# Performance work log

Hardware: AMD Instinct MI355X
Metric: run time of the kernel (lower is better)

## Reference

```python
import jax, jax.numpy as jnp
import numpy as np

B, C, N = 4, 192, 4096
K = 16                      # avg degree
E = B * N * K               # 262144 edges
C_OUT = 384


def setup_inputs() -> dict:
    key = jax.random.key(0)
    k1, k2, k3, k4 = jax.random.split(key, 4)
    x = jax.random.normal(k1, (B, C, N, 1), dtype=jnp.float32)
    edge_index = jax.random.randint(k2, (2, E), 0, B * N, dtype=jnp.int64)
    # BasicConv([2C, C_OUT]): 1x1 Conv2d + bias + ReLU (norm=None)
    W = jax.random.normal(k3, (C_OUT, 2 * C), dtype=jnp.float32) * (1.0 / np.sqrt(2 * C))
    b = jax.random.normal(k4, (C_OUT,), dtype=jnp.float32) * 0.01
    return {"x": x, "edge_index": edge_index, "W": W, "b": b}


def reference(x, edge_index, W, b):
    Bs, Cs, Ns, _ = x.shape
    BN = Bs * Ns
    # (B,C,N,1) -> flattened node table (B*N, C); node id = b*N + n
    x_flat = jnp.transpose(x[..., 0], (0, 2, 1)).reshape(BN, Cs)
    x_i = x_flat[edge_index[0]]          # (E, C) gather at dst
    x_j = x_flat[edge_index[1]]          # (E, C) gather at src
    diff = x_j - x_i
    # scatter-max over dst nodes; torch_scatter fills empty segments with 0
    agg = jax.ops.segment_max(diff, edge_index[0], num_segments=BN)
    agg = jnp.where(jnp.isfinite(agg), agg, 0.0)
    x_j_out = jnp.transpose(agg.reshape(Bs, Ns, Cs), (0, 2, 1))[..., None]  # (B,C,N,1)
    # interleave channels: cat along new axis 2 then reshape -> (B, 2C, N, 1)
    cat = jnp.stack([x, x_j_out], axis=2).reshape(Bs, 2 * Cs, Ns, 1)
    # 1x1 conv == GEMM over channels, + bias + ReLU
    out = jnp.einsum('oc,bcnw->bonw', W, cat) + b[None, :, None, None]
    return jax.nn.relu(out)
```

## Files before the change

### kernel.cpp

```cpp
#include <hip/hip_runtime.h>
#include <hip/hip_bf16.h>
#include <math.h>

#define Bz    4
#define Cch   192
#define Nn    4096
#define BN    16384
#define Ecnt  262144
#define COUT  384
#define CAP   64
#define MSTR  200

typedef __attribute__((ext_vector_type(8))) short short8;
typedef __attribute__((ext_vector_type(4))) float floatx4;

__device__ __forceinline__ float b2f(unsigned short u) {
    union { unsigned int i; float f; } z; z.i = ((unsigned int)u) << 16; return z.f;
}
__device__ __forceinline__ unsigned short f2b(float f) {
    __hip_bfloat16 h = __float2bfloat16(f);
    return *(unsigned short*)&h;
}

#define RED8(mm, FLD) do {                                                    \
    float a_ = fmaxf(fmaxf(b2f(v[0].FLD), b2f(v[1].FLD)),                     \
                     fmaxf(b2f(v[2].FLD), b2f(v[3].FLD)));                    \
    float b_ = fmaxf(fmaxf(b2f(v[4].FLD), b2f(v[5].FLD)),                     \
                     fmaxf(b2f(v[6].FLD), b2f(v[7].FLD)));                    \
    mm = fmaxf(mm, fmaxf(a_, b_)); } while (0)

__global__ __launch_bounds__(256) void prep_kernel(
    const float* __restrict__ x, const unsigned int* __restrict__ ew,
    const float* __restrict__ W, __hip_bfloat16* __restrict__ xb,
    __hip_bfloat16* __restrict__ Wxa, __hip_bfloat16* __restrict__ Wa,
    int* __restrict__ deg, int* __restrict__ flag) {
    int bid = blockIdx.x;
    if (bid < 3072) {
        __shared__ float tile[32][33];
        int b = bid / 768;
        int r = bid - b * 768;
        int c0 = (r >> 7) * 32;
        int n0 = (r & 127) * 32;
        int tx = threadIdx.x & 31, ty = threadIdx.x >> 5;
        for (int i = ty; i < 32; i += 8)
            tile[i][tx] = x[((size_t)(b * Cch + c0 + i)) * Nn + n0 + tx];
        __syncthreads();
        for (int i = ty; i < 32; i += 8)
            xb[((size_t)(b * Nn + n0 + i)) * Cch + c0 + tx] =
                __float2bfloat16(tile[tx][i]);
    } else if (bid < 3360) {
        int i = (bid - 3072) * 256 + threadIdx.x;
        int o = i / Cch, c = i - o * Cch;
        float wx = W[o * 2 * Cch + 2 * c];
        float wa = W[o * 2 * Cch + 2 * c + 1];
        Wxa[i] = __float2bfloat16(wx - wa);
        Wa[i]  = __float2bfloat16(wa);
    } else if (bid < 3424) {
        deg[(bid - 3360) * 256 + threadIdx.x] = 0;
    } else {
        __shared__ int s;
        if (threadIdx.x == 0) s = 1;
        __syncthreads();
        if (ew[2 * threadIdx.x + 1] != 0u) atomicAnd(&s, 0);
        __syncthreads();
        if (threadIdx.x == 0) *flag = s;
    }
}

__global__ __launch_bounds__(256) void fill_kernel(
    const int* __restrict__ ew, const int* __restrict__ flag,
    int* __restrict__ deg, int* __restrict__ slots) {
    int t = blockIdx.x * 256 + threadIdx.x;
    int d0, d1, s0, s1;
    if (*flag) {
        int4 dv = *(const int4*)&ew[4 * t];
        int4 sv = *(const int4*)&ew[2 * Ecnt + 4 * t];
        d0 = dv.x; d1 = dv.z; s0 = sv.x; s1 = sv.z;
    } else {
        int2 dv = *(const int2*)&ew[2 * t];
        int2 sv = *(const int2*)&ew[Ecnt + 2 * t];
        d0 = dv.x; d1 = dv.y; s0 = sv.x; s1 = sv.y;
    }
    int p0 = atomicAdd(&deg[d0], 1); if (p0 < CAP) slots[(d0 << 6) + p0] = s0;
    int p1 = atomicAdd(&deg[d1], 1); if (p1 < CAP) slots[(d1 << 6) + p1] = s1;
}

#define MFMA6()                                                                \
    acc00 = __builtin_amdgcn_mfma_f32_16x16x32_bf16(b0, af0, acc00, 0, 0, 0);  \
    acc10 = __builtin_amdgcn_mfma_f32_16x16x32_bf16(b0, af1, acc10, 0, 0, 0);  \
    acc01 = __builtin_amdgcn_mfma_f32_16x16x32_bf16(b1, af0, acc01, 0, 0, 0);  \
    acc11 = __builtin_amdgcn_mfma_f32_16x16x32_bf16(b1, af1, acc11, 0, 0, 0);  \
    acc02 = __builtin_amdgcn_mfma_f32_16x16x32_bf16(b2, af0, acc02, 0, 0, 0);  \
    acc12 = __builtin_amdgcn_mfma_f32_16x16x32_bf16(b2, af1, acc12, 0, 0, 0)

__global__ __launch_bounds__(512, 4) void p2_kernel(
    const int* __restrict__ deg, const int* __restrict__ slots,
    const __hip_bfloat16* __restrict__ xb,
    const __hip_bfloat16* __restrict__ Wxa, const __hip_bfloat16* __restrict__ Wa,
    const float* __restrict__ bias, float* __restrict__ out)
{
    __shared__ __align__(16) unsigned short Xs[32 * MSTR];
    __shared__ __align__(16) unsigned short Ms[32 * MSTR];
    int tid = threadIdx.x, bid = blockIdx.x;
    int lane = tid & 63, wave = tid >> 6;
    int quad = lane >> 4, lrow = lane & 15;
    int node0 = bid * 32;
    const unsigned short* xbu = (const unsigned short*)xb;
    int act = lane < 48;
    int cb = lane * 4;

    for (int nl = wave * 4; nl < wave * 4 + 4; nl++) {
        int node = node0 + nl;
        int d = deg[node]; if (d > CAP) d = CAP;
        d = __builtin_amdgcn_readfirstlane(d);
        int nbrval = 0;
        if (lane < d) nbrval = slots[(node << 6) + lane];
        ushort4 xv = {0, 0, 0, 0};
        if (act) xv = *(const ushort4*)&xbu[node * Cch + cb];
        float m0 = -INFINITY, m1 = -INFINITY, m2 = -INFINITY, m3 = -INFINITY;
        int k = 0;
        for (; k + 8 <= d; k += 8) {
            int s[8];
#pragma unroll
            for (int u = 0; u < 8; u++) s[u] = __builtin_amdgcn_readlane(nbrval, k + u);
            if (act) {
                ushort4 v[8];
#pragma unroll
                for (int u = 0; u < 8; u++) v[u] = *(const ushort4*)&xbu[s[u] * Cch + cb];
                RED8(m0, x); RED8(m1, y); RED8(m2, z); RED8(m3, w);
            }
        }
        if (k + 4 <= d) {
            int s0 = __builtin_amdgcn_readlane(nbrval, k);
            int s1 = __builtin_amdgcn_readlane(nbrval, k + 1);
            int s2 = __builtin_amdgcn_readlane(nbrval, k + 2);
            int s3 = __builtin_amdgcn_readlane(nbrval, k + 3);
            if (act) {
                ushort4 v0 = *(const ushort4*)&xbu[s0 * Cch + cb];
                ushort4 v1 = *(const ushort4*)&xbu[s1 * Cch + cb];
                ushort4 v2 = *(const ushort4*)&xbu[s2 * Cch + cb];
                ushort4 v3 = *(const ushort4*)&xbu[s3 * Cch + cb];
                m0 = fmaxf(m0, fmaxf(fmaxf(b2f(v0.x), b2f(v1.x)), fmaxf(b2f(v2.x), b2f(v3.x))));
                m1 = fmaxf(m1, fmaxf(fmaxf(b2f(v0.y), b2f(v1.y)), fmaxf(b2f(v2.y), b2f(v3.y))));
                m2 = fmaxf(m2, fmaxf(fmaxf(b2f(v0.z), b2f(v1.z)), fmaxf(b2f(v2.z), b2f(v3.z))));
                m3 = fmaxf(m3, fmaxf(fmaxf(b2f(v0.w), b2f(v1.w)), fmaxf(b2f(v2.w), b2f(v3.w))));
            }
            k += 4;
        }
        for (; k < d; k++) {
            int s = __builtin_amdgcn_readlane(nbrval, k);
            if (act) {
                ushort4 v = *(const ushort4*)&xbu[s * Cch + cb];
                m0 = fmaxf(m0, b2f(v.x)); m1 = fmaxf(m1, b2f(v.y));
                m2 = fmaxf(m2, b2f(v.z)); m3 = fmaxf(m3, b2f(v.w));
            }
        }
        if (act) {
            *(ushort4*)&Xs[nl * MSTR + cb] = xv;
            ushort4 o4;
            if (d > 0) {
                o4.x = f2b(m0); o4.y = f2b(m1); o4.z = f2b(m2); o4.w = f2b(m3);
            } else {
                o4 = xv;
            }
            *(ushort4*)&Ms[nl * MSTR + cb] = o4;
        }
    }
    __syncthreads();

    floatx4 acc00 = {}, acc01 = {}, acc02 = {}, acc10 = {}, acc11 = {}, acc12 = {};
    const unsigned short* Wx16 = (const unsigned short*)Wxa;
    const unsigned short* Wa16 = (const unsigned short*)Wa;
    size_t w0 = (size_t)(wave * 48 +  0 + lrow) * Cch;
    size_t w1 = (size_t)(wave * 48 + 16 + lrow) * Cch;
    size_t w2 = (size_t)(wave * 48 + 32 + lrow) * Cch;
    int kq = quad * 8;

    short8 b0 = *(const short8*)&Wx16[w0 + kq];
    short8 b1 = *(const short8*)&Wx16[w1 + kq];
    short8 b2 = *(const short8*)&Wx16[w2 + kq];
#pragma unroll
    for (int s = 0; s < 12; s++) {
        short8 n0, n1, n2;
        if (s < 11) {
            int sn = s + 1;
            const unsigned short* Wn = (sn >= 6) ? Wa16 : Wx16;
            int kkn = ((sn >= 6) ? sn - 6 : sn) * 32 + kq;
            n0 = *(const short8*)&Wn[w0 + kkn];
            n1 = *(const short8*)&Wn[w1 + kkn];
            n2 = *(const short8*)&Wn[w2 + kkn];
        }
        int kk = ((s >= 6) ? s - 6 : s) * 32 + kq;
        const unsigned short* Ar = (s >= 6) ? Ms : Xs;
        short8 af0 = *(const short8*)&Ar[lrow * MSTR + kk];
        short8 af1 = *(const short8*)&Ar[(16 + lrow) * MSTR + kk];
        MFMA6();
        if (s < 11) { b0 = n0; b1 = n1; b2 = n2; }
    }

    floatx4 accs[2][3] = {{acc00, acc01, acc02}, {acc10, acc11, acc12}};
#pragma unroll
    for (int i = 0; i < 2; i++) {
        int node = node0 + i * 16 + lrow;
        int b = node >> 12, n = node & 4095;
#pragma unroll
        for (int j = 0; j < 3; j++) {
            int ob = wave * 48 + j * 16 + quad * 4;
#pragma unroll
            for (int r = 0; r < 4; r++) {
                int o = ob + r;
                float v = accs[i][j][r] + bias[o];
                out[((size_t)(b * COUT + o)) * Nn + n] = fmaxf(v, 0.0f);
            }
        }
    }
}

extern "C" void kernel_launch(void* const* d_in, const int* in_sizes, int n_in,
                              void* d_out, int out_size, void* d_ws, size_t ws_size,
                              hipStream_t stream) {
    const float* x    = (const float*)d_in[0];
    const int*   ew   = (const int*)d_in[1];
    const float* W    = (const float*)d_in[2];
    const float* bias = (const float*)d_in[3];
    float* out        = (float*)d_out;

    char* ws = (char*)d_ws;
    __hip_bfloat16* xb   = (__hip_bfloat16*)ws;
    __hip_bfloat16* Wxa  = (__hip_bfloat16*)(ws + 12582912);
    __hip_bfloat16* Wa   = (__hip_bfloat16*)(ws + 12730368);
    int* deg   = (int*)(ws + 12877824);
    int* slots = (int*)(ws + 12943360);
    int* flag  = (int*)(ws + 17137664);

    prep_kernel<<<3425, 256, 0, stream>>>(x, (const unsigned int*)ew, W, xb, Wxa, Wa, deg, flag);
    fill_kernel<<<Ecnt / 512, 256, 0, stream>>>(ew, flag, deg, slots);
    p2_kernel<<<BN / 32, 512, 0, stream>>>(deg, slots, xb, Wxa, Wa, bias, out);
}
```

Baseline: 123.2 us.

## Halve nodes per block, prefetch neighbor lists, pick edge dtype on host

The fused gather-max plus GEMM kernel now handles 16 nodes per block instead of 32, doubling the grid to 1024 blocks with half the LDS and a single MFMA row tile per wave. Each wave loads both nodes' degree and neighbor lists up front, so those latencies overlap before the gather loop starts. The on-device int64/int32 flag detection is replaced by a host-side check on the input byte size, which selects a specialised fill kernel and removes the flag read and its branch. The trade-off is that every block now reloads the full weight matrix for only 16 nodes, doubling weight traffic per output.

```diff
diff --git a/kernel.cpp b/kernel.cpp
--- a/kernel.cpp
+++ b/kernel.cpp
@@ -30,10 +30,9 @@
     mm = fmaxf(mm, fmaxf(a_, b_)); } while (0)
 
 __global__ __launch_bounds__(256) void prep_kernel(
-    const float* __restrict__ x, const unsigned int* __restrict__ ew,
-    const float* __restrict__ W, __hip_bfloat16* __restrict__ xb,
-    __hip_bfloat16* __restrict__ Wxa, __hip_bfloat16* __restrict__ Wa,
-    int* __restrict__ deg, int* __restrict__ flag) {
+    const float* __restrict__ x, const float* __restrict__ W,
+    __hip_bfloat16* __restrict__ xb, __hip_bfloat16* __restrict__ Wxa,
+    __hip_bfloat16* __restrict__ Wa, int* __restrict__ deg) {
     int bid = blockIdx.x;
     if (bid < 3072) {
         __shared__ float tile[32][33];
@@ -55,43 +54,35 @@
         float wa = W[o * 2 * Cch + 2 * c + 1];
         Wxa[i] = __float2bfloat16(wx - wa);
         Wa[i]  = __float2bfloat16(wa);
-    } else if (bid < 3424) {
+    } else {
         deg[(bid - 3360) * 256 + threadIdx.x] = 0;
-    } else {
-        __shared__ int s;
-        if (threadIdx.x == 0) s = 1;
-        __syncthreads();
-        if (ew[2 * threadIdx.x + 1] != 0u) atomicAnd(&s, 0);
-        __syncthreads();
-        if (threadIdx.x == 0) *flag = s;
-    }
-}
-
-__global__ __launch_bounds__(256) void fill_kernel(
-    const int* __restrict__ ew, const int* __restrict__ flag,
-    int* __restrict__ deg, int* __restrict__ slots) {
-    int t = blockIdx.x * 256 + threadIdx.x;
-    int d0, d1, s0, s1;
-    if (*flag) {
-        int4 dv = *(const int4*)&ew[4 * t];
-        int4 sv = *(const int4*)&ew[2 * Ecnt + 4 * t];
-        d0 = dv.x; d1 = dv.z; s0 = sv.x; s1 = sv.z;
-    } else {
-        int2 dv = *(const int2*)&ew[2 * t];
-        int2 sv = *(const int2*)&ew[Ecnt + 2 * t];
-        d0 = dv.x; d1 = dv.y; s0 = sv.x; s1 = sv.y;
-    }
+    }
+}
+
+__device__ __forceinline__ void fill_body(
+    int d0, int d1, int s0, int s1, int* deg, int* slots) {
     int p0 = atomicAdd(&deg[d0], 1); if (p0 < CAP) slots[(d0 << 6) + p0] = s0;
     int p1 = atomicAdd(&deg[d1], 1); if (p1 < CAP) slots[(d1 << 6) + p1] = s1;
 }
-
-#define MFMA6()                                                                \
-    acc00 = __builtin_amdgcn_mfma_f32_16x16x32_bf16(b0, af0, acc00, 0, 0, 0);  \
-    acc10 = __builtin_amdgcn_mfma_f32_16x16x32_bf16(b0, af1, acc10, 0, 0, 0);  \
-    acc01 = __builtin_amdgcn_mfma_f32_16x16x32_bf16(b1, af0, acc01, 0, 0, 0);  \
-    acc11 = __builtin_amdgcn_mfma_f32_16x16x32_bf16(b1, af1, acc11, 0, 0, 0);  \
-    acc02 = __builtin_amdgcn_mfma_f32_16x16x32_bf16(b2, af0, acc02, 0, 0, 0);  \
-    acc12 = __builtin_amdgcn_mfma_f32_16x16x32_bf16(b2, af1, acc12, 0, 0, 0)
+__global__ __launch_bounds__(256) void fill64_kernel(
+    const int* __restrict__ ew, int* __restrict__ deg, int* __restrict__ slots) {
+    int t = blockIdx.x * 256 + threadIdx.x;
+    int4 dv = *(const int4*)&ew[4 * t];
+    int4 sv = *(const int4*)&ew[2 * Ecnt + 4 * t];
+    fill_body(dv.x, dv.z, sv.x, sv.z, deg, slots);
+}
+__global__ __launch_bounds__(256) void fill32_kernel(
+    const int* __restrict__ ew, int* __restrict__ deg, int* __restrict__ slots) {
+    int t = blockIdx.x * 256 + threadIdx.x;
+    int2 dv = *(const int2*)&ew[2 * t];
+    int2 sv = *(const int2*)&ew[Ecnt + 2 * t];
+    fill_body(dv.x, dv.y, sv.x, sv.y, deg, slots);
+}
+
+#define MFMA3()                                                                \
+    acc0 = __builtin_amdgcn_mfma_f32_16x16x32_bf16(b0, af0, acc0, 0, 0, 0);    \
+    acc1 = __builtin_amdgcn_mfma_f32_16x16x32_bf16(b1, af0, acc1, 0, 0, 0);    \
+    acc2 = __builtin_amdgcn_mfma_f32_16x16x32_bf16(b2, af0, acc2, 0, 0, 0)
 
 __global__ __launch_bounds__(512, 4) void p2_kernel(
     const int* __restrict__ deg, const int* __restrict__ slots,
@@ -99,22 +90,29 @@
     const __hip_bfloat16* __restrict__ Wxa, const __hip_bfloat16* __restrict__ Wa,
     const float* __restrict__ bias, float* __restrict__ out)
 {
-    __shared__ __align__(16) unsigned short Xs[32 * MSTR];
-    __shared__ __align__(16) unsigned short Ms[32 * MSTR];
+    __shared__ __align__(16) unsigned short Xs[16 * MSTR];
+    __shared__ __align__(16) unsigned short Ms[16 * MSTR];
     int tid = threadIdx.x, bid = blockIdx.x;
     int lane = tid & 63, wave = tid >> 6;
     int quad = lane >> 4, lrow = lane & 15;
-    int node0 = bid * 32;
+    int node0 = bid * 16;
     const unsigned short* xbu = (const unsigned short*)xb;
     int act = lane < 48;
     int cb = lane * 4;
 
-    for (int nl = wave * 4; nl < wave * 4 + 4; nl++) {
+    int dd[2], nbr[2];
+#pragma unroll
+    for (int q = 0; q < 2; q++) {
+        int node = node0 + wave * 2 + q;
+        int d = deg[node]; if (d > CAP) d = CAP;
+        dd[q] = __builtin_amdgcn_readfirstlane(d);
+        nbr[q] = (lane < dd[q]) ? slots[(node << 6) + lane] : 0;
+    }
+#pragma unroll
+    for (int q = 0; q < 2; q++) {
+        int nl = wave * 2 + q;
         int node = node0 + nl;
-        int d = deg[node]; if (d > CAP) d = CAP;
-        d = __builtin_amdgcn_readfirstlane(d);
-        int nbrval = 0;
-        if (lane < d) nbrval = slots[(node << 6) + lane];
+        int d = dd[q], nbrval = nbr[q];
         ushort4 xv = {0, 0, 0, 0};
         if (act) xv = *(const ushort4*)&xbu[node * Cch + cb];
         float m0 = -INFINITY, m1 = -INFINITY, m2 = -INFINITY, m3 = -INFINITY;
@@ -168,7 +166,7 @@
     }
     __syncthreads();
 
-    floatx4 acc00 = {}, acc01 = {}, acc02 = {}, acc10 = {}, acc11 = {}, acc12 = {};
+    floatx4 acc0 = {}, acc1 = {}, acc2 = {};
     const unsigned short* Wx16 = (const unsigned short*)Wxa;
     const unsigned short* Wa16 = (const unsigned short*)Wa;
     size_t w0 = (size_t)(wave * 48 +  0 + lrow) * Cch;
@@ -193,25 +191,21 @@
         int kk = ((s >= 6) ? s - 6 : s) * 32 + kq;
         const unsigned short* Ar = (s >= 6) ? Ms : Xs;
         short8 af0 = *(const short8*)&Ar[lrow * MSTR + kk];
-        short8 af1 = *(const short8*)&Ar[(16 + lrow) * MSTR + kk];
-        MFMA6();
+        MFMA3();
         if (s < 11) { b0 = n0; b1 = n1; b2 = n2; }
     }
 
-    floatx4 accs[2][3] = {{acc00, acc01, acc02}, {acc10, acc11, acc12}};
-#pragma unroll
-    for (int i = 0; i < 2; i++) {
-        int node = node0 + i * 16 + lrow;
-        int b = node >> 12, n = node & 4095;
-#pragma unroll
-        for (int j = 0; j < 3; j++) {
-            int ob = wave * 48 + j * 16 + quad * 4;
-#pragma unroll
-            for (int r = 0; r < 4; r++) {
-                int o = ob + r;
-                float v = accs[i][j][r] + bias[o];
-                out[((size_t)(b * COUT + o)) * Nn + n] = fmaxf(v, 0.0f);
-            }
+    floatx4 accs[3] = {acc0, acc1, acc2};
+    int node = node0 + lrow;
+    int b = node >> 12, n = node & 4095;
+#pragma unroll
+    for (int j = 0; j < 3; j++) {
+        int ob = wave * 48 + j * 16 + quad * 4;
+#pragma unroll
+        for (int r = 0; r < 4; r++) {
+            int o = ob + r;
+            float v = accs[j][r] + bias[o];
+            out[((size_t)(b * COUT + o)) * Nn + n] = fmaxf(v, 0.0f);
         }
     }
 }
@@ -231,9 +225,13 @@
     __hip_bfloat16* Wa   = (__hip_bfloat16*)(ws + 12730368);
     int* deg   = (int*)(ws + 12877824);
     int* slots = (int*)(ws + 12943360);
-    int* flag  = (int*)(ws + 17137664);
-
-    prep_kernel<<<3425, 256, 0, stream>>>(x, (const unsigned int*)ew, W, xb, Wxa, Wa, deg, flag);
-    fill_kernel<<<Ecnt / 512, 256, 0, stream>>>(ew, flag, deg, slots);
-    p2_kernel<<<BN / 32, 512, 0, stream>>>(deg, slots, xb, Wxa, Wa, bias, out);
-}
+
+    bool is64 = (in_sizes[1] >= (int)(2u * Ecnt * 8u));
+
+    prep_kernel<<<3424, 256, 0, stream>>>(x, W, xb, Wxa, Wa, deg);
+    if (is64)
+        fill64_kernel<<<Ecnt / 512, 256, 0, stream>>>(ew, deg, slots);
+    else
+        fill32_kernel<<<Ecnt / 512, 256, 0, stream>>>(ew, deg, slots);
+    p2_kernel<<<BN / 16, 512, 0, stream>>>(deg, slots, xb, Wxa, Wa, bias, out);
+}
```

After: 135.2 us. 9.8% more time.
